# Optimization experiments

Hardware: AMD Instinct MI355X
Metric: run time of the kernel (lower is better)

## Reference

```python
import jax, jax.numpy as jnp
import numpy as np

N_NODES = 100000
N_EDGES = 1600000
N_GRAPHS = 512
IN_CH = 64
HID = 64
OUT_CH = 2
NC = 3


def setup_inputs() -> dict:
    key = jax.random.key(0)
    ks = jax.random.split(key, 10)
    x = jax.random.normal(ks[0], (N_NODES, IN_CH), dtype=jnp.float32)
    edge_index = jax.random.randint(ks[1], (2, N_EDGES), 0, N_NODES, dtype=jnp.int64)
    batch = jnp.sort(jax.random.randint(ks[2], (N_NODES,), 0, N_GRAPHS, dtype=jnp.int64))
    s = 1.0 / np.sqrt(HID)
    W_rel = jax.random.normal(ks[3], (NC, HID, HID), dtype=jnp.float32) * s
    W_root = jax.random.normal(ks[4], (NC, HID, HID), dtype=jnp.float32) * s
    b_conv = jax.random.normal(ks[5], (NC, HID), dtype=jnp.float32) * s
    W1 = jax.random.normal(ks[6], (HID, 2 * HID), dtype=jnp.float32) * s
    b1 = jax.random.normal(ks[7], (2 * HID,), dtype=jnp.float32) * s
    W2 = jax.random.normal(ks[8], (2 * HID, OUT_CH), dtype=jnp.float32) * (1.0 / np.sqrt(2 * HID))
    b2 = jax.random.normal(ks[9], (OUT_CH,), dtype=jnp.float32) * (1.0 / np.sqrt(2 * HID))
    return {"x": x, "edge_index": edge_index, "batch": batch,
            "W_rel": W_rel, "W_root": W_root, "b_conv": b_conv,
            "W1": W1, "b1": b1, "W2": W2, "b2": b2}


def reference(x, edge_index, batch, W_rel, W_root, b_conv, W1, b1, W2, b2):
    src, dst = edge_index[0], edge_index[1]
    h = x
    for i in range(NC):
        # PyG GraphConv(aggr='add'): lin_rel(scatter_add(h[src] -> dst)) + lin_root(h)
        agg = jax.ops.segment_sum(h[src], dst, num_segments=N_NODES)  # [N, HID]
        h = jax.nn.relu(agg @ W_rel[i] + b_conv[i] + h @ W_root[i])
    pooled = jax.ops.segment_sum(h, batch, num_segments=N_GRAPHS)  # [G, HID]
    # MLP readout [HID, 2*HID, OUT]
    out = jax.nn.sigmoid(jax.nn.relu(pooled @ W1 + b1) @ W2 + b2)  # [G, OUT]
    return out, pooled
```

## Files before the change

### kernel.cpp

```cpp
#include <hip/hip_runtime.h>
#include <math.h>

#define N_NODES 100000
#define N_EDGES 1600000
#define N_GRAPHS 512
#define HID 64
#define NC 3

#define NBUCK 782
#define EPB 8192
#define NPBLK 196
#define BSTRIDE 4096
#define DUMMY N_NODES

typedef unsigned int uint;

__device__ __forceinline__ ushort f2bf(float f) {
    uint u = __float_as_uint(f);
    u += 0x7fffu + ((u >> 16) & 1u);
    return (ushort)(u >> 16);
}
__device__ __forceinline__ uint packbf2(float a, float b) {
    return (uint)f2bf(a) | ((uint)f2bf(b) << 16);
}


__global__ __launch_bounds__(256) void chist_kernel(const int* __restrict__ dst,
                                                    int* __restrict__ cbins) {
    __shared__ int bins[NBUCK];
    for (int i = threadIdx.x; i < NBUCK; i += 256) bins[i] = 0;
    __syncthreads();
    int start = blockIdx.x * EPB;
    int endd = min(start + EPB, N_EDGES);
    for (int e = start + threadIdx.x; e < endd; e += 256)
        atomicAdd(&bins[dst[e] >> 7], 1);
    __syncthreads();
    for (int i = threadIdx.x; i < NBUCK; i += 256)
        if (bins[i]) atomicAdd(&cbins[i], bins[i]);
}

__global__ __launch_bounds__(1024) void cscan_kernel(const int* __restrict__ cbins,
                                                     int* __restrict__ cstart,
                                                     int* __restrict__ ccursor) {
    __shared__ int s[1024];
    int t = threadIdx.x;
    int v = (t < NBUCK) ? cbins[t] : 0;
    int val = v;
    s[t] = val;
    __syncthreads();
    for (int off = 1; off < 1024; off <<= 1) {
        int o = (t >= off) ? s[t - off] : 0;
        __syncthreads();
        val += o;
        s[t] = val;
        __syncthreads();
    }
    if (t < NBUCK) {
        int ex = val - v;
        cstart[t] = ex;
        ccursor[t] = ex;
    }
    if (t == 0) cstart[NBUCK] = N_EDGES;
}

__global__ __launch_bounds__(256) void partition_kernel(const int* __restrict__ src,
                                                        const int* __restrict__ dst,
                                                        int* __restrict__ ccursor,
                                                        int2* __restrict__ part) {
    __shared__ int cnt[NBUCK];
    __shared__ int base[NBUCK];
    __shared__ int cur[NBUCK];
    for (int i = threadIdx.x; i < NBUCK; i += 256) { cnt[i] = 0; cur[i] = 0; }
    __syncthreads();
    int start = blockIdx.x * EPB;
    int endd = min(start + EPB, N_EDGES);
    for (int e = start + threadIdx.x; e < endd; e += 256)
        atomicAdd(&cnt[dst[e] >> 7], 1);
    __syncthreads();
    for (int i = threadIdx.x; i < NBUCK; i += 256)
        base[i] = cnt[i] ? atomicAdd(&ccursor[i], cnt[i]) : 0;
    __syncthreads();
    for (int e = start + threadIdx.x; e < endd; e += 256) {
        int d = dst[e];
        int b = d >> 7;
        int r = atomicAdd(&cur[b], 1);
        part[base[b] + r] = make_int2(src[e], d);
    }
}

__global__ __launch_bounds__(256) void bcsr_kernel(const int2* __restrict__ part,
                                                   const int* __restrict__ cstart,
                                                   int* __restrict__ row_ptr,
                                                   int* __restrict__ pdeg,
                                                   int* __restrict__ col) {
    __shared__ int deg[128];
    __shared__ int cur[128];
    __shared__ int pre[128];
    __shared__ int ss[256];
    int b = blockIdx.x;
    int t = threadIdx.x;
    int s0 = cstart[b], s1 = cstart[b + 1];
    if (t < 128) { deg[t] = 0; cur[t] = 0; }
    __syncthreads();
    for (int e = s0 + t; e < s1; e += 256)
        atomicAdd(&deg[part[e].y & 127], 1);
    __syncthreads();
    int v = (t < 128) ? ((deg[t] + 7) & ~7) : 0;
    int val = v;
    ss[t] = val;
    __syncthreads();
    for (int off = 1; off < 256; off <<= 1) {
        int o = (t >= off) ? ss[t - off] : 0;
        __syncthreads();
        val += o;
        ss[t] = val;
        __syncthreads();
    }
    if (t < 128) pre[t] = val - v;
    __syncthreads();
    int base = b * BSTRIDE;
    int node = b * 128 + t;
    if (t < 128 && node < N_NODES) {
        row_ptr[node] = base + pre[t];
        pdeg[node] = v;
    }
    for (int e = s0 + t; e < s1; e += 256) {
        int2 p = part[e];
        int nl = p.y & 127;
        int r = atomicAdd(&cur[nl], 1);
        col[base + pre[nl] + r] = p.x;
    }
    __syncthreads();
    if (t < 128) {
        for (int i = deg[t]; i < v; i++)
            col[base + pre[t] + i] = DUMMY;
    }
}


__global__ __launch_bounds__(256) void cvt_kernel(const float* __restrict__ x,
                                                  ushort* __restrict__ hX) {
    int i = blockIdx.x * blockDim.x + threadIdx.x;
    int stride = gridDim.x * blockDim.x;
    const float4* x4 = (const float4*)x;
    for (; i < N_NODES * HID / 4; i += stride) {
        float4 v = x4[i];
        uint2 o;
        o.x = packbf2(v.x, v.y);
        o.y = packbf2(v.z, v.w);
        *(uint2*)(hX + (size_t)i * 4) = o;
    }
}


__global__ __launch_bounds__(256) void wprep_kernel(const float* __restrict__ W_rel,
                                                    const float* __restrict__ W_root,
                                                    ushort* __restrict__ WT) {
    int i = blockIdx.x * blockDim.x + threadIdx.x;
    if (i >= NC * 2 * HID * HID) return;
    int l = i / (2 * HID * HID);
    int rem = i % (2 * HID * HID);
    int m = rem / (HID * HID);
    int j = rem % (HID * HID);
    int colc = j / HID;
    int k = j % HID;
    const float* W = (m ? W_root : W_rel) + l * HID * HID;
    WT[i] = f2bf(W[k * HID + colc]);
}


#define ACC4(A, v) { A.x += __uint_as_float((v).x << 16); \
                     A.y += __uint_as_float((v).x & 0xffff0000u); \
                     A.z += __uint_as_float((v).y << 16); \
                     A.w += __uint_as_float((v).y & 0xffff0000u); }

__global__ __launch_bounds__(256) void gather_kernel(
    const ushort* __restrict__ hin, ushort* __restrict__ agg,
    const int* __restrict__ row_ptr, const int* __restrict__ pdeg,
    const int* __restrict__ col)
{
    int lane = threadIdx.x & 63;
    int slot = lane >> 4;
    int ch   = (lane & 15) * 4;
    int gwid = (blockIdx.x * blockDim.x + threadIdx.x) >> 6;
    int nwaves = (gridDim.x * blockDim.x) >> 6;

    for (int n0 = gwid * 4; n0 < N_NODES; n0 += nwaves * 4) {
        int n = n0 + slot;
        const int* row = col + row_ptr[n];
        int pd = pdeg[n];
        float4 a0 = {0.f,0.f,0.f,0.f}, a1 = {0.f,0.f,0.f,0.f};
        float4 a2 = {0.f,0.f,0.f,0.f}, a3 = {0.f,0.f,0.f,0.f};
        for (int e = 0; e < pd; e += 8) {
            int4 ca = *(const int4*)(row + e);
            int4 cb = *(const int4*)(row + e + 4);
            uint2 v0 = *(const uint2*)(hin + (size_t)ca.x * HID + ch);
            uint2 v1 = *(const uint2*)(hin + (size_t)ca.y * HID + ch);
            uint2 v2 = *(const uint2*)(hin + (size_t)ca.z * HID + ch);
            uint2 v3 = *(const uint2*)(hin + (size_t)ca.w * HID + ch);
            uint2 v4 = *(const uint2*)(hin + (size_t)cb.x * HID + ch);
            uint2 v5 = *(const uint2*)(hin + (size_t)cb.y * HID + ch);
            uint2 v6 = *(const uint2*)(hin + (size_t)cb.z * HID + ch);
            uint2 v7 = *(const uint2*)(hin + (size_t)cb.w * HID + ch);
            ACC4(a0, v0); ACC4(a1, v1); ACC4(a2, v2); ACC4(a3, v3);
            ACC4(a0, v4); ACC4(a1, v5); ACC4(a2, v6); ACC4(a3, v7);
        }
        a0.x += a1.x + a2.x + a3.x;
        a0.y += a1.y + a2.y + a3.y;
        a0.z += a1.z + a2.z + a3.z;
        a0.w += a1.w + a2.w + a3.w;
        uint2 o;
        o.x = packbf2(a0.x, a0.y);
        o.y = packbf2(a0.z, a0.w);
        *(uint2*)(agg + (size_t)n * HID + ch) = o;
    }
}


__global__ __launch_bounds__(256) void transform_kernel(
    const ushort* __restrict__ hin, const ushort* __restrict__ agg,
    ushort* __restrict__ hout, const ushort* __restrict__ WTl,
    const float* __restrict__ bias)
{
    typedef __attribute__((ext_vector_type(8))) short short8;
    typedef __attribute__((ext_vector_type(4))) float f32x4;
    __shared__ float lds[4][16][68];
    int lane = threadIdx.x & 63;
    int wid  = threadIdx.x >> 6;
    int mrow = lane & 15;
    int kg   = lane >> 4;
    int gw = (blockIdx.x * blockDim.x + threadIdx.x) >> 6;
    int nw = (gridDim.x * blockDim.x) >> 6;

    short8 Bf[4][4];
#pragma unroll
    for (int c = 0; c < 4; c++)
#pragma unroll
        for (int m = 0; m < 2; m++)
#pragma unroll
            for (int h = 0; h < 2; h++)
                Bf[c][m * 2 + h] = *(const short8*)(
                    WTl + m * HID * HID + (c * 16 + mrow) * HID + h * 32 + kg * 8);

    float bv[4];
#pragma unroll
    for (int c = 0; c < 4; c++) bv[c] = bias[c * 16 + mrow];

    for (int ng = gw; ng < N_NODES / 16; ng += nw) {
        size_t rb = ((size_t)ng * 16 + mrow) * HID + kg * 8;
        short8 Ah0 = *(const short8*)(hin + rb);
        short8 Ah1 = *(const short8*)(hin + rb + 32);
        short8 Aa0 = *(const short8*)(agg + rb);
        short8 Aa1 = *(const short8*)(agg + rb + 32);
#pragma unroll
        for (int c = 0; c < 4; c++) {
            f32x4 acc = {0.f, 0.f, 0.f, 0.f};
            acc = __builtin_amdgcn_mfma_f32_16x16x32_bf16(Aa0, Bf[c][0], acc, 0, 0, 0);
            acc = __builtin_amdgcn_mfma_f32_16x16x32_bf16(Aa1, Bf[c][1], acc, 0, 0, 0);
            acc = __builtin_amdgcn_mfma_f32_16x16x32_bf16(Ah0, Bf[c][2], acc, 0, 0, 0);
            acc = __builtin_amdgcn_mfma_f32_16x16x32_bf16(Ah1, Bf[c][3], acc, 0, 0, 0);
#pragma unroll
            for (int r = 0; r < 4; r++)
                lds[wid][kg * 4 + r][c * 16 + mrow] = fmaxf(acc[r] + bv[c], 0.f);
        }
        asm volatile("s_waitcnt lgkmcnt(0)" ::: "memory");
        const float* lr = &lds[wid][mrow][kg * 16];
        float4 f0 = *(const float4*)(lr + 0);
        float4 f1 = *(const float4*)(lr + 4);
        float4 f2 = *(const float4*)(lr + 8);
        float4 f3 = *(const float4*)(lr + 12);
        uint4 o0, o1;
        o0.x = packbf2(f0.x, f0.y); o0.y = packbf2(f0.z, f0.w);
        o0.z = packbf2(f1.x, f1.y); o0.w = packbf2(f1.z, f1.w);
        o1.x = packbf2(f2.x, f2.y); o1.y = packbf2(f2.z, f2.w);
        o1.z = packbf2(f3.x, f3.y); o1.w = packbf2(f3.z, f3.w);
        ushort* orow = hout + ((size_t)ng * 16 + mrow) * HID + kg * 16;
        *(uint4*)(orow) = o0;
        *(uint4*)(orow + 8) = o1;
    }
}


__global__ __launch_bounds__(256) void pool_kernel(
    const ushort* __restrict__ h, const int* __restrict__ batch,
    float* __restrict__ pooled_ws) {
    const int CH = 64;
    int lane = threadIdx.x & 63;
    int gwid = (blockIdx.x * blockDim.x + threadIdx.x) >> 6;
    int n0 = gwid * CH;
    if (n0 >= N_NODES) return;
    int nend = min(n0 + CH, N_NODES);
    int cur = batch[n0];
    float acc = 0.f;
    for (int n = n0; n < nend; n++) {
        int g = batch[n];
        if (g != cur) {
            atomicAdd(&pooled_ws[cur * HID + lane], acc);
            acc = 0.f;
            cur = g;
        }
        acc += __uint_as_float(((uint)h[(size_t)n * HID + lane]) << 16);
    }
    atomicAdd(&pooled_ws[cur * HID + lane], acc);
}


__global__ void mlp_kernel(const float* __restrict__ pooled_ws,
                           const float* __restrict__ W1, const float* __restrict__ b1,
                           const float* __restrict__ W2, const float* __restrict__ b2,
                           float* __restrict__ out, float* __restrict__ pooled_out) {
    __shared__ float sp[HID];
    __shared__ float red[4];
    int g = blockIdx.x, t = threadIdx.x;
    if (t < HID) {
        float v = pooled_ws[g * HID + t];
        sp[t] = v;
        pooled_out[g * HID + t] = v;
    }
    __syncthreads();
    float acc = b1[t];
#pragma unroll
    for (int k = 0; k < HID; k++) acc = fmaf(sp[k], W1[k * 128 + t], acc);
    float hid = fmaxf(acc, 0.f);
    float p0 = hid * W2[t * 2 + 0];
    float p1 = hid * W2[t * 2 + 1];
    for (int off = 32; off > 0; off >>= 1) {
        p0 += __shfl_down(p0, off, 64);
        p1 += __shfl_down(p1, off, 64);
    }
    int wave = t >> 6, lane = t & 63;
    if (lane == 0) { red[wave * 2 + 0] = p0; red[wave * 2 + 1] = p1; }
    __syncthreads();
    if (t == 0) {
        float o0 = red[0] + red[2] + b2[0];
        float o1 = red[1] + red[3] + b2[1];
        out[g * 2 + 0] = 1.f / (1.f + expf(-o0));
        out[g * 2 + 1] = 1.f / (1.f + expf(-o1));
    }
}


extern "C" void kernel_launch(void* const* d_in, const int* in_sizes, int n_in,
                              void* d_out, int out_size, void* d_ws, size_t ws_size,
                              hipStream_t stream) {
    const float* x      = (const float*)d_in[0];
    const int*   ei     = (const int*)d_in[1];
    const int*   batch  = (const int*)d_in[2];
    const float* W_rel  = (const float*)d_in[3];
    const float* W_root = (const float*)d_in[4];
    const float* b_conv = (const float*)d_in[5];
    const float* W1     = (const float*)d_in[6];
    const float* b1     = (const float*)d_in[7];
    const float* W2     = (const float*)d_in[8];
    const float* b2     = (const float*)d_in[9];

    float* outp       = (float*)d_out;
    float* pooled_out = (float*)d_out + N_GRAPHS * 2;

    const size_t HROWS_B = ((size_t)(N_NODES + 1) * HID * 2 + 255) & ~(size_t)255;

    char* ws = (char*)d_ws;
    size_t off = 0;
    ushort* hX = (ushort*)(ws + off); off += HROWS_B;
    ushort* hA = (ushort*)(ws + off); off += HROWS_B;
    ushort* hB = (ushort*)(ws + off); off += HROWS_B;
    ushort* gg = (ushort*)(ws + off); off += ((size_t)N_NODES * HID * 2 + 255) & ~(size_t)255;
    ushort* WT = (ushort*)(ws + off); off += ((size_t)NC * 2 * HID * HID * 2 + 255) & ~(size_t)255;
    int2* part    = (int2*)(ws + off); off += (size_t)N_EDGES * 8;
    int* colidx   = (int*)(ws + off); off += (size_t)NBUCK * BSTRIDE * 4;
    int* row_ptr  = (int*)(ws + off); off += (size_t)(N_NODES + 4) * 4;
    int* pdeg     = (int*)(ws + off); off += (size_t)(N_NODES + 4) * 4;
    int* cbins    = (int*)(ws + off); off += (size_t)NBUCK * 4;
    int* cstart   = (int*)(ws + off); off += (size_t)(NBUCK + 4) * 4;
    int* ccursor  = (int*)(ws + off); off += (size_t)NBUCK * 4;
    float* pooled_ws = (float*)(ws + off); off += (size_t)N_GRAPHS * HID * 4;

    const int* esrc = ei;
    const int* edst = ei + N_EDGES;

    hipMemsetAsync(cbins, 0, (size_t)NBUCK * 4, stream);
    hipMemsetAsync(pooled_ws, 0, (size_t)N_GRAPHS * HID * 4, stream);
    hipMemsetAsync(hX + (size_t)N_NODES * HID, 0, HID * 2, stream);
    hipMemsetAsync(hA + (size_t)N_NODES * HID, 0, HID * 2, stream);
    hipMemsetAsync(hB + (size_t)N_NODES * HID, 0, HID * 2, stream);

    cvt_kernel<<<2048, 256, 0, stream>>>(x, hX);
    wprep_kernel<<<(NC * 2 * HID * HID + 255) / 256, 256, 0, stream>>>(W_rel, W_root, WT);

    chist_kernel<<<NPBLK, 256, 0, stream>>>(edst, cbins);
    cscan_kernel<<<1, 1024, 0, stream>>>(cbins, cstart, ccursor);
    partition_kernel<<<NPBLK, 256, 0, stream>>>(esrc, edst, ccursor, part);
    bcsr_kernel<<<NBUCK, 256, 0, stream>>>(part, cstart, row_ptr, pdeg, colidx);

    gather_kernel<<<2048, 256, 0, stream>>>(hX, gg, row_ptr, pdeg, colidx);
    transform_kernel<<<512, 256, 0, stream>>>(hX, gg, hA, WT + 0 * 2 * HID * HID, b_conv + 0 * HID);
    gather_kernel<<<2048, 256, 0, stream>>>(hA, gg, row_ptr, pdeg, colidx);
    transform_kernel<<<512, 256, 0, stream>>>(hA, gg, hB, WT + 1 * 2 * HID * HID, b_conv + 1 * HID);
    gather_kernel<<<2048, 256, 0, stream>>>(hB, gg, row_ptr, pdeg, colidx);
    transform_kernel<<<512, 256, 0, stream>>>(hB, gg, hA, WT + 2 * 2 * HID * HID, b_conv + 2 * HID);

    pool_kernel<<<391, 256, 0, stream>>>(hA, batch, pooled_ws);
    mlp_kernel<<<N_GRAPHS, 128, 0, stream>>>(pooled_ws, W1, b1, W2, b2, outp, pooled_out);
}
```

Baseline: 336.8 us.

## Replace histogram+scan bucketing with fixed-stride bucket slots in partition

Removes the separate histogram and scan kernels by giving each destination bucket a fixed-capacity slot region (PSTRIDE entries), so partition blocks reserve space with atomics on a zeroed cursor array. bcsr reads each bucket's count directly from the cursor. Edge loads are vectorized as int4 and the block count is doubled to raise parallelism. The fixed capacity assumes no bucket exceeds 3072 edges (about 2048 expected), which would overflow for adversarial inputs.

```diff
diff --git a/kernel.cpp b/kernel.cpp
--- a/kernel.cpp
+++ b/kernel.cpp
@@ -8,8 +8,9 @@
 #define NC 3
 
 #define NBUCK 782
-#define EPB 8192
-#define NPBLK 196
+#define EPB 4096
+#define NPBLK 391
+#define PSTRIDE 3072
 #define BSTRIDE 4096
 #define DUMMY N_NODES
 
@@ -24,44 +25,6 @@
     return (uint)f2bf(a) | ((uint)f2bf(b) << 16);
 }
 
-
-__global__ __launch_bounds__(256) void chist_kernel(const int* __restrict__ dst,
-                                                    int* __restrict__ cbins) {
-    __shared__ int bins[NBUCK];
-    for (int i = threadIdx.x; i < NBUCK; i += 256) bins[i] = 0;
-    __syncthreads();
-    int start = blockIdx.x * EPB;
-    int endd = min(start + EPB, N_EDGES);
-    for (int e = start + threadIdx.x; e < endd; e += 256)
-        atomicAdd(&bins[dst[e] >> 7], 1);
-    __syncthreads();
-    for (int i = threadIdx.x; i < NBUCK; i += 256)
-        if (bins[i]) atomicAdd(&cbins[i], bins[i]);
-}
-
-__global__ __launch_bounds__(1024) void cscan_kernel(const int* __restrict__ cbins,
-                                                     int* __restrict__ cstart,
-                                                     int* __restrict__ ccursor) {
-    __shared__ int s[1024];
-    int t = threadIdx.x;
-    int v = (t < NBUCK) ? cbins[t] : 0;
-    int val = v;
-    s[t] = val;
-    __syncthreads();
-    for (int off = 1; off < 1024; off <<= 1) {
-        int o = (t >= off) ? s[t - off] : 0;
-        __syncthreads();
-        val += o;
-        s[t] = val;
-        __syncthreads();
-    }
-    if (t < NBUCK) {
-        int ex = val - v;
-        cstart[t] = ex;
-        ccursor[t] = ex;
-    }
-    if (t == 0) cstart[NBUCK] = N_EDGES;
-}
 
 __global__ __launch_bounds__(256) void partition_kernel(const int* __restrict__ src,
                                                         const int* __restrict__ dst,
@@ -72,24 +35,34 @@
     __shared__ int cur[NBUCK];
     for (int i = threadIdx.x; i < NBUCK; i += 256) { cnt[i] = 0; cur[i] = 0; }
     __syncthreads();
-    int start = blockIdx.x * EPB;
-    int endd = min(start + EPB, N_EDGES);
-    for (int e = start + threadIdx.x; e < endd; e += 256)
-        atomicAdd(&cnt[dst[e] >> 7], 1);
+    const int4* d4 = (const int4*)dst;
+    const int4* s4 = (const int4*)src;
+    int i0 = blockIdx.x * (EPB / 4);
+    int i1 = min(i0 + EPB / 4, N_EDGES / 4);
+    for (int i = i0 + threadIdx.x; i < i1; i += 256) {
+        int4 d = d4[i];
+        atomicAdd(&cnt[d.x >> 7], 1);
+        atomicAdd(&cnt[d.y >> 7], 1);
+        atomicAdd(&cnt[d.z >> 7], 1);
+        atomicAdd(&cnt[d.w >> 7], 1);
+    }
     __syncthreads();
     for (int i = threadIdx.x; i < NBUCK; i += 256)
-        base[i] = cnt[i] ? atomicAdd(&ccursor[i], cnt[i]) : 0;
-    __syncthreads();
-    for (int e = start + threadIdx.x; e < endd; e += 256) {
-        int d = dst[e];
-        int b = d >> 7;
-        int r = atomicAdd(&cur[b], 1);
-        part[base[b] + r] = make_int2(src[e], d);
-    }
-}
+        base[i] = cnt[i] ? (i * PSTRIDE + atomicAdd(&ccursor[i], cnt[i])) : 0;
+    __syncthreads();
+    for (int i = i0 + threadIdx.x; i < i1; i += 256) {
+        int4 d = d4[i];
+        int4 s = s4[i];
+        int b0 = d.x >> 7; part[base[b0] + atomicAdd(&cur[b0], 1)] = make_int2(s.x, d.x);
+        int b1 = d.y >> 7; part[base[b1] + atomicAdd(&cur[b1], 1)] = make_int2(s.y, d.y);
+        int b2 = d.z >> 7; part[base[b2] + atomicAdd(&cur[b2], 1)] = make_int2(s.z, d.z);
+        int b3 = d.w >> 7; part[base[b3] + atomicAdd(&cur[b3], 1)] = make_int2(s.w, d.w);
+    }
+}
+
 
 __global__ __launch_bounds__(256) void bcsr_kernel(const int2* __restrict__ part,
-                                                   const int* __restrict__ cstart,
+                                                   const int* __restrict__ ccursor,
                                                    int* __restrict__ row_ptr,
                                                    int* __restrict__ pdeg,
                                                    int* __restrict__ col) {
@@ -99,7 +72,8 @@
     __shared__ int ss[256];
     int b = blockIdx.x;
     int t = threadIdx.x;
-    int s0 = cstart[b], s1 = cstart[b + 1];
+    int s0 = b * PSTRIDE;
+    int s1 = s0 + ccursor[b];
     if (t < 128) { deg[t] = 0; cur[t] = 0; }
     __syncthreads();
     for (int e = s0 + t; e < s1; e += 256)
@@ -366,19 +340,17 @@
     ushort* hB = (ushort*)(ws + off); off += HROWS_B;
     ushort* gg = (ushort*)(ws + off); off += ((size_t)N_NODES * HID * 2 + 255) & ~(size_t)255;
     ushort* WT = (ushort*)(ws + off); off += ((size_t)NC * 2 * HID * HID * 2 + 255) & ~(size_t)255;
-    int2* part    = (int2*)(ws + off); off += (size_t)N_EDGES * 8;
+    int2* part    = (int2*)(ws + off); off += (size_t)NBUCK * PSTRIDE * 8;
     int* colidx   = (int*)(ws + off); off += (size_t)NBUCK * BSTRIDE * 4;
     int* row_ptr  = (int*)(ws + off); off += (size_t)(N_NODES + 4) * 4;
     int* pdeg     = (int*)(ws + off); off += (size_t)(N_NODES + 4) * 4;
-    int* cbins    = (int*)(ws + off); off += (size_t)NBUCK * 4;
-    int* cstart   = (int*)(ws + off); off += (size_t)(NBUCK + 4) * 4;
     int* ccursor  = (int*)(ws + off); off += (size_t)NBUCK * 4;
     float* pooled_ws = (float*)(ws + off); off += (size_t)N_GRAPHS * HID * 4;
 
     const int* esrc = ei;
     const int* edst = ei + N_EDGES;
 
-    hipMemsetAsync(cbins, 0, (size_t)NBUCK * 4, stream);
+    hipMemsetAsync(ccursor, 0, (size_t)NBUCK * 4, stream);
     hipMemsetAsync(pooled_ws, 0, (size_t)N_GRAPHS * HID * 4, stream);
     hipMemsetAsync(hX + (size_t)N_NODES * HID, 0, HID * 2, stream);
     hipMemsetAsync(hA + (size_t)N_NODES * HID, 0, HID * 2, stream);
@@ -387,10 +359,8 @@
     cvt_kernel<<<2048, 256, 0, stream>>>(x, hX);
     wprep_kernel<<<(NC * 2 * HID * HID + 255) / 256, 256, 0, stream>>>(W_rel, W_root, WT);
 
-    chist_kernel<<<NPBLK, 256, 0, stream>>>(edst, cbins);
-    cscan_kernel<<<1, 1024, 0, stream>>>(cbins, cstart, ccursor);
     partition_kernel<<<NPBLK, 256, 0, stream>>>(esrc, edst, ccursor, part);
-    bcsr_kernel<<<NBUCK, 256, 0, stream>>>(part, cstart, row_ptr, pdeg, colidx);
+    bcsr_kernel<<<NBUCK, 256, 0, stream>>>(part, ccursor, row_ptr, pdeg, colidx);
 
     gather_kernel<<<2048, 256, 0, stream>>>(hX, gg, row_ptr, pdeg, colidx);
     transform_kernel<<<512, 256, 0, stream>>>(hX, gg, hA, WT + 0 * 2 * HID * HID, b_conv + 0 * HID);
```

New measurement: 306.1 us. 1.1x faster.
